# Performance work log

Hardware: AMD Instinct MI355X
Metric: run time of the kernel (lower is better)

The kernel has to match this reference:

```python
import jax, jax.numpy as jnp
import numpy as np

MARGIN = 0.3
HARD_FACTOR = 0.0
EPS = 1e-6


def setup_inputs() -> dict:
    key = jax.random.key(0)
    k1, k2 = jax.random.split(key)
    inputs = jax.random.normal(k1, (4096, 256), dtype=jnp.float32)
    targets = jax.random.randint(k2, (4096,), 0, 512, dtype=jnp.int64)
    return {"inputs": inputs, "targets": targets}


def reference(inputs, targets):
    n = inputs.shape[0]
    half = n // 2
    # L2-normalize features (matches normalize(): x / (||x|| + 1e-6))
    x = inputs / (jnp.linalg.norm(inputs, axis=-1, keepdims=True) + EPS)
    # pairwise euclidean distances, clamped at 1e-6 before sqrt
    sq = jnp.sum(x * x, axis=1)                      # (n,)
    dist = sq[:, None] + sq[None, :] - 2.0 * (x @ x.T)  # (n, n)
    dist = jnp.sqrt(jnp.clip(dist, EPS))
    # same-identity mask
    mask = targets[:, None] == targets[None, :]      # (n, n) bool
    # rows in the first half mine over columns [half:n], rows in the
    # second half mine over columns [0:half] -> gather the opposite half
    first = (jnp.arange(n) < half)[:, None]          # (n, 1)
    d_o = jnp.where(first, dist[:, half:], dist[:, :half])  # (n, half)
    m_o = jnp.where(first, mask[:, half:], mask[:, :half])  # (n, half) bool
    pos_any = jnp.any(m_o, axis=1)
    neg_any = jnp.any(~m_o, axis=1)
    dist_ap = jnp.where(pos_any,
                        jnp.max(jnp.where(m_o, d_o, -jnp.inf), axis=1),
                        0.0)
    dist_an = jnp.where(neg_any,
                        jnp.min(jnp.where(m_o, jnp.inf, d_o), axis=1),
                        1.0)
    dist_ap = dist_ap * (1.0 + HARD_FACTOR)
    dist_an = dist_an * (1.0 - HARD_FACTOR)
    # MarginRankingLoss(margin)(dist_an, dist_ap, y=1) =
    #   mean(relu(-(dist_an - dist_ap) + margin))
    loss = jnp.mean(jax.nn.relu(dist_ap - dist_an + MARGIN))
    return loss
```

## Files before the change

kernel.cpp:

```cpp
#include <hip/hip_runtime.h>
#include <math.h>

#define N 4096
#define D 256
#define HALF 2048
#define MARGIN 0.3f

#define BM 64

typedef __attribute__((ext_vector_type(8))) short bf16x8;
typedef __attribute__((ext_vector_type(4))) float f32x4;

typedef __attribute__((address_space(1))) const unsigned int gas_uint;
typedef __attribute__((address_space(3))) unsigned int las_uint;

__device__ __forceinline__ void gld16(const unsigned short* g, unsigned short* l) {
    __builtin_amdgcn_global_load_lds((gas_uint*)g, (las_uint*)l, 16, 0, 0);
}

__device__ __forceinline__ unsigned short f2bf(float x) {
    unsigned int u = __float_as_uint(x);
    return (unsigned short)((u + 0x7fffu + ((u >> 16) & 1u)) >> 16);
}

__global__ __launch_bounds__(256) void k_norm(const float* __restrict__ in,
                                              unsigned short* __restrict__ xnb,
                                              float* __restrict__ sq,
                                              int* __restrict__ ap,
                                              int* __restrict__ an) {
    const int row = blockIdx.x * 4 + (threadIdx.x >> 6);
    const int lane = threadIdx.x & 63;
    const float4 v = *(const float4*)&in[(size_t)row * D + lane * 4];
    float s = v.x * v.x + v.y * v.y + v.z * v.z + v.w * v.w;
#pragma unroll
    for (int o = 1; o < 64; o <<= 1) s += __shfl_xor(s, o, 64);
    float nrm = sqrtf(s);
    float inv = 1.0f / (nrm + 1e-6f);
    ushort4 o4;
    o4.x = f2bf(v.x * inv);
    o4.y = f2bf(v.y * inv);
    o4.z = f2bf(v.z * inv);
    o4.w = f2bf(v.w * inv);
    *(ushort4*)&xnb[(size_t)row * D + lane * 4] = o4;
    if (lane == 0) {
        float q = nrm * inv;
        sq[row] = q * q;
        ap[row] = 0;
        an[row] = 0x7f800000;
    }
}

__global__ __launch_bounds__(256, 2) void k_tile(const unsigned short* __restrict__ xnb,
                                                 const float* __restrict__ sq,
                                                 const int* __restrict__ tg,
                                                 int* __restrict__ ap,
                                                 int* __restrict__ an) {
    __shared__ unsigned short As[BM * D];
    __shared__ unsigned short Bs[BM * D];

    const int bi = blockIdx.y, bj = blockIdx.x;
    const int I0 = bi * BM;
    const int J0 = bj * BM;
    const int tid = threadIdx.x;
    const int wave = tid >> 6, lane = tid & 63;
    const int wm = wave >> 1, wn = wave & 1;
    const int lrow = lane & 15, lquad = lane >> 4;

    const unsigned short* Ag = xnb + (size_t)I0 * D;
    const unsigned short* Bg = xnb + (size_t)(HALF + J0) * D;

#pragma unroll
    for (int i = 0; i < 8; ++i) {
        const int ch = i * 4 + wave;
        const int e = ch * 64 + lane;
        const int row = e >> 5;
        const int sc = (e & 31) ^ (row & 7);
        gld16(Ag + row * D + sc * 8, &As[ch * 512]);
        gld16(Bg + row * D + sc * 8, &Bs[ch * 512]);
    }
    asm volatile("s_waitcnt vmcnt(0)" ::: "memory");
    __syncthreads();

    f32x4 acc[2][2];
#pragma unroll
    for (int a = 0; a < 2; ++a)
#pragma unroll
        for (int b = 0; b < 2; ++b) acc[a][b] = (f32x4){0.f, 0.f, 0.f, 0.f};

#pragma unroll
    for (int kk = 0; kk < 8; ++kk) {
        bf16x8 af[2], bfr[2];
#pragma unroll
        for (int mi = 0; mi < 2; ++mi) {
            const int r = wm * 32 + mi * 16 + lrow;
            const int s = r * 32 + ((kk * 4 + lquad) ^ (r & 7));
            af[mi] = *(const bf16x8*)&As[s * 8];
        }
#pragma unroll
        for (int nj = 0; nj < 2; ++nj) {
            const int r = wn * 32 + nj * 16 + lrow;
            const int s = r * 32 + ((kk * 4 + lquad) ^ (r & 7));
            bfr[nj] = *(const bf16x8*)&Bs[s * 8];
        }
#pragma unroll
        for (int mi = 0; mi < 2; ++mi)
#pragma unroll
            for (int nj = 0; nj < 2; ++nj)
                acc[mi][nj] = __builtin_amdgcn_mfma_f32_16x16x32_bf16(
                    af[mi], bfr[nj], acc[mi][nj], 0, 0, 0);
    }

    float sqi[2][4], sqj[2];
    int tgi[2][4], tgj[2];
#pragma unroll
    for (int mi = 0; mi < 2; ++mi)
#pragma unroll
        for (int r = 0; r < 4; ++r) {
            int gi = I0 + wm * 32 + mi * 16 + lquad * 4 + r;
            sqi[mi][r] = sq[gi];
            tgi[mi][r] = tg[gi];
        }
#pragma unroll
    for (int nj = 0; nj < 2; ++nj) {
        int gj = HALF + J0 + wn * 32 + nj * 16 + lrow;
        sqj[nj] = sq[gj];
        tgj[nj] = tg[gj];
    }

    const float INF = __int_as_float(0x7f800000);
    float rap[2][4], ran[2][4], capv[2], canv[2];
#pragma unroll
    for (int mi = 0; mi < 2; ++mi)
#pragma unroll
        for (int r = 0; r < 4; ++r) { rap[mi][r] = 0.f; ran[mi][r] = INF; }
#pragma unroll
    for (int nj = 0; nj < 2; ++nj) { capv[nj] = 0.f; canv[nj] = INF; }

#pragma unroll
    for (int mi = 0; mi < 2; ++mi)
#pragma unroll
        for (int nj = 0; nj < 2; ++nj)
#pragma unroll
            for (int r = 0; r < 4; ++r) {
                float d2 = sqi[mi][r] + sqj[nj] - 2.0f * acc[mi][nj][r];
                float d = sqrtf(fmaxf(d2, 1e-6f));
                if (tgi[mi][r] == tgj[nj]) {
                    rap[mi][r] = fmaxf(rap[mi][r], d);
                    capv[nj] = fmaxf(capv[nj], d);
                } else {
                    ran[mi][r] = fminf(ran[mi][r], d);
                    canv[nj] = fminf(canv[nj], d);
                }
            }

#pragma unroll
    for (int mi = 0; mi < 2; ++mi)
#pragma unroll
        for (int r = 0; r < 4; ++r) {
#pragma unroll
            for (int o = 1; o < 16; o <<= 1) {
                rap[mi][r] = fmaxf(rap[mi][r], __shfl_xor(rap[mi][r], o, 64));
                ran[mi][r] = fminf(ran[mi][r], __shfl_xor(ran[mi][r], o, 64));
            }
        }
#pragma unroll
    for (int nj = 0; nj < 2; ++nj) {
#pragma unroll
        for (int o = 16; o < 64; o <<= 1) {
            capv[nj] = fmaxf(capv[nj], __shfl_xor(capv[nj], o, 64));
            canv[nj] = fminf(canv[nj], __shfl_xor(canv[nj], o, 64));
        }
    }

    int* sra = (int*)As;
    int* srn = sra + BM;
    int* sca = srn + BM;
    int* scn = sca + BM;

    __syncthreads();
    if (tid < BM) { sra[tid] = 0; srn[tid] = 0x7f800000;
                    sca[tid] = 0; scn[tid] = 0x7f800000; }
    __syncthreads();
    if (lrow == 0) {
#pragma unroll
        for (int mi = 0; mi < 2; ++mi)
#pragma unroll
            for (int r = 0; r < 4; ++r) {
                int lr = wm * 32 + mi * 16 + lquad * 4 + r;
                atomicMax(&sra[lr], __float_as_int(rap[mi][r]));
                atomicMin(&srn[lr], __float_as_int(ran[mi][r]));
            }
    }
    if (lquad == 0) {
#pragma unroll
        for (int nj = 0; nj < 2; ++nj) {
            int lc = wn * 32 + nj * 16 + lrow;
            atomicMax(&sca[lc], __float_as_int(capv[nj]));
            atomicMin(&scn[lc], __float_as_int(canv[nj]));
        }
    }
    __syncthreads();
    if (tid < BM) {
        atomicMax(&ap[I0 + tid], sra[tid]);
        atomicMin(&an[I0 + tid], srn[tid]);
        atomicMax(&ap[HALF + J0 + tid], sca[tid]);
        atomicMin(&an[HALF + J0 + tid], scn[tid]);
    }
}

__global__ __launch_bounds__(1024) void k_loss(const int* __restrict__ ap,
                                               const int* __restrict__ an,
                                               float* __restrict__ out) {
    const int t = threadIdx.x;
    float s = 0.f;
#pragma unroll
    for (int i = t; i < N; i += 1024) {
        float dap = __int_as_float(ap[i]);
        int anb = an[i];
        float dan = (anb == 0x7f800000) ? 1.0f : __int_as_float(anb);
        float v = dap - dan + MARGIN;
        s += (v > 0.f) ? v : 0.f;
    }
#pragma unroll
    for (int o = 32; o > 0; o >>= 1) s += __shfl_down(s, o, 64);
    __shared__ float wsum[16];
    if ((t & 63) == 0) wsum[t >> 6] = s;
    __syncthreads();
    if (t == 0) {
        float tot = 0.f;
#pragma unroll
        for (int w = 0; w < 16; ++w) tot += wsum[w];
        out[0] = tot / (float)N;
    }
}

extern "C" void kernel_launch(void* const* d_in, const int* in_sizes, int n_in,
                              void* d_out, int out_size, void* d_ws, size_t ws_size,
                              hipStream_t stream) {
    const float* in = (const float*)d_in[0];
    const int* tg = (const int*)d_in[1];
    float* out = (float*)d_out;

    unsigned short* xnb = (unsigned short*)d_ws;
    float* sq = (float*)(xnb + (size_t)N * D);
    int* ap = (int*)(sq + N);
    int* an = ap + N;

    k_norm<<<N / 4, 256, 0, stream>>>(in, xnb, sq, ap, an);
    k_tile<<<dim3(HALF / BM, HALF / BM), 256, 0, stream>>>(xnb, sq, tg, ap, an);
    k_loss<<<1, 1024, 0, stream>>>(ap, an, out);
}
```

Baseline: 73.47 us.

## Fuse norm, tile and loss into one cooperative persistent kernel

Merges the three kernels into one cooperative kernel with 256 persistent blocks separated by grid syncs. Each block processes four tile jobs and writes its per-tile row and column partial max/min into partial buffers instead of using global atomics. A final phase reduces those partials and the per-block loss sums. This removes two kernel launches and global atomic contention, at the cost of grid-sync overhead, larger workspace traffic and fewer concurrent blocks per tile.

```diff
diff --git a/kernel.cpp b/kernel.cpp
--- a/kernel.cpp
+++ b/kernel.cpp
@@ -1,5 +1,8 @@
 #include <hip/hip_runtime.h>
+#include <hip/hip_cooperative_groups.h>
 #include <math.h>
+
+namespace cg = cooperative_groups;
 
 #define N 4096
 #define D 256
@@ -7,6 +10,9 @@
 #define MARGIN 0.3f
 
 #define BM 64
+#define GRID 256
+#define TPB 256
+#define NTJ 32
 
 typedef __attribute__((ext_vector_type(8))) short bf16x8;
 typedef __attribute__((ext_vector_type(4))) float f32x4;
@@ -23,213 +29,231 @@
     return (unsigned short)((u + 0x7fffu + ((u >> 16) & 1u)) >> 16);
 }
 
-__global__ __launch_bounds__(256) void k_norm(const float* __restrict__ in,
-                                              unsigned short* __restrict__ xnb,
-                                              float* __restrict__ sq,
-                                              int* __restrict__ ap,
-                                              int* __restrict__ an) {
-    const int row = blockIdx.x * 4 + (threadIdx.x >> 6);
-    const int lane = threadIdx.x & 63;
-    const float4 v = *(const float4*)&in[(size_t)row * D + lane * 4];
-    float s = v.x * v.x + v.y * v.y + v.z * v.z + v.w * v.w;
-#pragma unroll
-    for (int o = 1; o < 64; o <<= 1) s += __shfl_xor(s, o, 64);
-    float nrm = sqrtf(s);
-    float inv = 1.0f / (nrm + 1e-6f);
-    ushort4 o4;
-    o4.x = f2bf(v.x * inv);
-    o4.y = f2bf(v.y * inv);
-    o4.z = f2bf(v.z * inv);
-    o4.w = f2bf(v.w * inv);
-    *(ushort4*)&xnb[(size_t)row * D + lane * 4] = o4;
-    if (lane == 0) {
-        float q = nrm * inv;
-        sq[row] = q * q;
-        ap[row] = 0;
-        an[row] = 0x7f800000;
-    }
-}
-
-__global__ __launch_bounds__(256, 2) void k_tile(const unsigned short* __restrict__ xnb,
-                                                 const float* __restrict__ sq,
-                                                 const int* __restrict__ tg,
-                                                 int* __restrict__ ap,
-                                                 int* __restrict__ an) {
+__global__ __launch_bounds__(TPB) void k_fused(const float* __restrict__ in,
+                                               const int* __restrict__ tg,
+                                               float* __restrict__ out,
+                                               unsigned short* __restrict__ xnb,
+                                               float* __restrict__ sq,
+                                               int* __restrict__ rp_ap,
+                                               int* __restrict__ rp_an,
+                                               int* __restrict__ cp_ap,
+                                               int* __restrict__ cp_an,
+                                               float* __restrict__ bsum) {
+    cg::grid_group grid = cg::this_grid();
+    const int tid = threadIdx.x;
+    const int wave = tid >> 6, lane = tid & 63;
+
+#pragma unroll
+    for (int r = 0; r < 4; ++r) {
+        const int row = blockIdx.x * 16 + wave * 4 + r;
+        const float4 v = *(const float4*)&in[(size_t)row * D + lane * 4];
+        float s = v.x * v.x + v.y * v.y + v.z * v.z + v.w * v.w;
+#pragma unroll
+        for (int o = 1; o < 64; o <<= 1) s += __shfl_xor(s, o, 64);
+        float nrm = sqrtf(s);
+        float inv = 1.0f / (nrm + 1e-6f);
+        ushort4 o4;
+        o4.x = f2bf(v.x * inv);
+        o4.y = f2bf(v.y * inv);
+        o4.z = f2bf(v.z * inv);
+        o4.w = f2bf(v.w * inv);
+        *(ushort4*)&xnb[(size_t)row * D + lane * 4] = o4;
+        if (lane == 0) {
+            float q = nrm * inv;
+            sq[row] = q * q;
+        }
+    }
+
+    grid.sync();
+
     __shared__ unsigned short As[BM * D];
     __shared__ unsigned short Bs[BM * D];
-
-    const int bi = blockIdx.y, bj = blockIdx.x;
-    const int I0 = bi * BM;
-    const int J0 = bj * BM;
-    const int tid = threadIdx.x;
-    const int wave = tid >> 6, lane = tid & 63;
+    __shared__ int sra[BM], srn[BM], sca[BM], scn[BM];
+
     const int wm = wave >> 1, wn = wave & 1;
     const int lrow = lane & 15, lquad = lane >> 4;
-
-    const unsigned short* Ag = xnb + (size_t)I0 * D;
-    const unsigned short* Bg = xnb + (size_t)(HALF + J0) * D;
-
-#pragma unroll
-    for (int i = 0; i < 8; ++i) {
-        const int ch = i * 4 + wave;
-        const int e = ch * 64 + lane;
-        const int row = e >> 5;
-        const int sc = (e & 31) ^ (row & 7);
-        gld16(Ag + row * D + sc * 8, &As[ch * 512]);
-        gld16(Bg + row * D + sc * 8, &Bs[ch * 512]);
-    }
-    asm volatile("s_waitcnt vmcnt(0)" ::: "memory");
-    __syncthreads();
-
-    f32x4 acc[2][2];
-#pragma unroll
-    for (int a = 0; a < 2; ++a)
-#pragma unroll
-        for (int b = 0; b < 2; ++b) acc[a][b] = (f32x4){0.f, 0.f, 0.f, 0.f};
-
-#pragma unroll
-    for (int kk = 0; kk < 8; ++kk) {
-        bf16x8 af[2], bfr[2];
-#pragma unroll
-        for (int mi = 0; mi < 2; ++mi) {
-            const int r = wm * 32 + mi * 16 + lrow;
-            const int s = r * 32 + ((kk * 4 + lquad) ^ (r & 7));
-            af[mi] = *(const bf16x8*)&As[s * 8];
-        }
+    const float INF = __int_as_float(0x7f800000);
+
+    for (int jt = 0; jt < 4; ++jt) {
+        const int job = jt * GRID + blockIdx.x;
+        const int bi = job >> 5, bj = job & (NTJ - 1);
+        const int I0 = bi * BM;
+        const int J0 = bj * BM;
+        const unsigned short* Ag = xnb + (size_t)I0 * D;
+        const unsigned short* Bg = xnb + (size_t)(HALF + J0) * D;
+
+        __syncthreads();
+#pragma unroll
+        for (int i = 0; i < 8; ++i) {
+            const int ch = i * 4 + wave;
+            const int e = ch * 64 + lane;
+            const int row = e >> 5;
+            const int sc = (e & 31) ^ (row & 7);
+            gld16(Ag + row * D + sc * 8, &As[ch * 512]);
+            gld16(Bg + row * D + sc * 8, &Bs[ch * 512]);
+        }
+        if (tid < BM) {
+            sra[tid] = 0; srn[tid] = 0x7f800000;
+            sca[tid] = 0; scn[tid] = 0x7f800000;
+        }
+        asm volatile("s_waitcnt vmcnt(0)" ::: "memory");
+        __syncthreads();
+
+        f32x4 acc[2][2];
+#pragma unroll
+        for (int a = 0; a < 2; ++a)
+#pragma unroll
+            for (int b = 0; b < 2; ++b) acc[a][b] = (f32x4){0.f, 0.f, 0.f, 0.f};
+
+#pragma unroll
+        for (int kk = 0; kk < 8; ++kk) {
+            bf16x8 af[2], bfr[2];
+#pragma unroll
+            for (int mi = 0; mi < 2; ++mi) {
+                const int r = wm * 32 + mi * 16 + lrow;
+                const int s = r * 32 + ((kk * 4 + lquad) ^ (r & 7));
+                af[mi] = *(const bf16x8*)&As[s * 8];
+            }
+#pragma unroll
+            for (int nj = 0; nj < 2; ++nj) {
+                const int r = wn * 32 + nj * 16 + lrow;
+                const int s = r * 32 + ((kk * 4 + lquad) ^ (r & 7));
+                bfr[nj] = *(const bf16x8*)&Bs[s * 8];
+            }
+#pragma unroll
+            for (int mi = 0; mi < 2; ++mi)
+#pragma unroll
+                for (int nj = 0; nj < 2; ++nj)
+                    acc[mi][nj] = __builtin_amdgcn_mfma_f32_16x16x32_bf16(
+                        af[mi], bfr[nj], acc[mi][nj], 0, 0, 0);
+        }
+
+        float sqi[2][4], sqj[2];
+        int tgi[2][4], tgj[2];
+#pragma unroll
+        for (int mi = 0; mi < 2; ++mi)
+#pragma unroll
+            for (int r = 0; r < 4; ++r) {
+                int gi = I0 + wm * 32 + mi * 16 + lquad * 4 + r;
+                sqi[mi][r] = sq[gi];
+                tgi[mi][r] = tg[gi];
+            }
 #pragma unroll
         for (int nj = 0; nj < 2; ++nj) {
-            const int r = wn * 32 + nj * 16 + lrow;
-            const int s = r * 32 + ((kk * 4 + lquad) ^ (r & 7));
-            bfr[nj] = *(const bf16x8*)&Bs[s * 8];
-        }
+            int gj = HALF + J0 + wn * 32 + nj * 16 + lrow;
+            sqj[nj] = sq[gj];
+            tgj[nj] = tg[gj];
+        }
+
+        float rap[2][4], ran[2][4], capv[2], canv[2];
+#pragma unroll
+        for (int mi = 0; mi < 2; ++mi)
+#pragma unroll
+            for (int r = 0; r < 4; ++r) { rap[mi][r] = 0.f; ran[mi][r] = INF; }
+#pragma unroll
+        for (int nj = 0; nj < 2; ++nj) { capv[nj] = 0.f; canv[nj] = INF; }
+
 #pragma unroll
         for (int mi = 0; mi < 2; ++mi)
 #pragma unroll
             for (int nj = 0; nj < 2; ++nj)
-                acc[mi][nj] = __builtin_amdgcn_mfma_f32_16x16x32_bf16(
-                    af[mi], bfr[nj], acc[mi][nj], 0, 0, 0);
-    }
-
-    float sqi[2][4], sqj[2];
-    int tgi[2][4], tgj[2];
-#pragma unroll
-    for (int mi = 0; mi < 2; ++mi)
-#pragma unroll
-        for (int r = 0; r < 4; ++r) {
-            int gi = I0 + wm * 32 + mi * 16 + lquad * 4 + r;
-            sqi[mi][r] = sq[gi];
-            tgi[mi][r] = tg[gi];
-        }
-#pragma unroll
-    for (int nj = 0; nj < 2; ++nj) {
-        int gj = HALF + J0 + wn * 32 + nj * 16 + lrow;
-        sqj[nj] = sq[gj];
-        tgj[nj] = tg[gj];
-    }
-
-    const float INF = __int_as_float(0x7f800000);
-    float rap[2][4], ran[2][4], capv[2], canv[2];
-#pragma unroll
-    for (int mi = 0; mi < 2; ++mi)
-#pragma unroll
-        for (int r = 0; r < 4; ++r) { rap[mi][r] = 0.f; ran[mi][r] = INF; }
-#pragma unroll
-    for (int nj = 0; nj < 2; ++nj) { capv[nj] = 0.f; canv[nj] = INF; }
-
-#pragma unroll
-    for (int mi = 0; mi < 2; ++mi)
-#pragma unroll
-        for (int nj = 0; nj < 2; ++nj)
+#pragma unroll
+                for (int r = 0; r < 4; ++r) {
+                    float d2 = sqi[mi][r] + sqj[nj] - 2.0f * acc[mi][nj][r];
+                    float d = sqrtf(fmaxf(d2, 1e-6f));
+                    if (tgi[mi][r] == tgj[nj]) {
+                        rap[mi][r] = fmaxf(rap[mi][r], d);
+                        capv[nj] = fmaxf(capv[nj], d);
+                    } else {
+                        ran[mi][r] = fminf(ran[mi][r], d);
+                        canv[nj] = fminf(canv[nj], d);
+                    }
+                }
+
+#pragma unroll
+        for (int mi = 0; mi < 2; ++mi)
 #pragma unroll
             for (int r = 0; r < 4; ++r) {
-                float d2 = sqi[mi][r] + sqj[nj] - 2.0f * acc[mi][nj][r];
-                float d = sqrtf(fmaxf(d2, 1e-6f));
-                if (tgi[mi][r] == tgj[nj]) {
-                    rap[mi][r] = fmaxf(rap[mi][r], d);
-                    capv[nj] = fmaxf(capv[nj], d);
-                } else {
-                    ran[mi][r] = fminf(ran[mi][r], d);
-                    canv[nj] = fminf(canv[nj], d);
+#pragma unroll
+                for (int o = 1; o < 16; o <<= 1) {
+                    rap[mi][r] = fmaxf(rap[mi][r], __shfl_xor(rap[mi][r], o, 64));
+                    ran[mi][r] = fminf(ran[mi][r], __shfl_xor(ran[mi][r], o, 64));
                 }
             }
-
-#pragma unroll
-    for (int mi = 0; mi < 2; ++mi)
-#pragma unroll
-        for (int r = 0; r < 4; ++r) {
-#pragma unroll
-            for (int o = 1; o < 16; o <<= 1) {
-                rap[mi][r] = fmaxf(rap[mi][r], __shfl_xor(rap[mi][r], o, 64));
-                ran[mi][r] = fminf(ran[mi][r], __shfl_xor(ran[mi][r], o, 64));
-            }
-        }
-#pragma unroll
-    for (int nj = 0; nj < 2; ++nj) {
-#pragma unroll
-        for (int o = 16; o < 64; o <<= 1) {
-            capv[nj] = fmaxf(capv[nj], __shfl_xor(capv[nj], o, 64));
-            canv[nj] = fminf(canv[nj], __shfl_xor(canv[nj], o, 64));
-        }
-    }
-
-    int* sra = (int*)As;
-    int* srn = sra + BM;
-    int* sca = srn + BM;
-    int* scn = sca + BM;
-
-    __syncthreads();
-    if (tid < BM) { sra[tid] = 0; srn[tid] = 0x7f800000;
-                    sca[tid] = 0; scn[tid] = 0x7f800000; }
-    __syncthreads();
-    if (lrow == 0) {
-#pragma unroll
-        for (int mi = 0; mi < 2; ++mi)
-#pragma unroll
-            for (int r = 0; r < 4; ++r) {
-                int lr = wm * 32 + mi * 16 + lquad * 4 + r;
-                atomicMax(&sra[lr], __float_as_int(rap[mi][r]));
-                atomicMin(&srn[lr], __float_as_int(ran[mi][r]));
-            }
-    }
-    if (lquad == 0) {
 #pragma unroll
         for (int nj = 0; nj < 2; ++nj) {
-            int lc = wn * 32 + nj * 16 + lrow;
-            atomicMax(&sca[lc], __float_as_int(capv[nj]));
-            atomicMin(&scn[lc], __float_as_int(canv[nj]));
-        }
-    }
-    __syncthreads();
-    if (tid < BM) {
-        atomicMax(&ap[I0 + tid], sra[tid]);
-        atomicMin(&an[I0 + tid], srn[tid]);
-        atomicMax(&ap[HALF + J0 + tid], sca[tid]);
-        atomicMin(&an[HALF + J0 + tid], scn[tid]);
-    }
-}
-
-__global__ __launch_bounds__(1024) void k_loss(const int* __restrict__ ap,
-                                               const int* __restrict__ an,
-                                               float* __restrict__ out) {
-    const int t = threadIdx.x;
-    float s = 0.f;
-#pragma unroll
-    for (int i = t; i < N; i += 1024) {
-        float dap = __int_as_float(ap[i]);
-        int anb = an[i];
+#pragma unroll
+            for (int o = 16; o < 64; o <<= 1) {
+                capv[nj] = fmaxf(capv[nj], __shfl_xor(capv[nj], o, 64));
+                canv[nj] = fminf(canv[nj], __shfl_xor(canv[nj], o, 64));
+            }
+        }
+
+        if (lrow == 0) {
+#pragma unroll
+            for (int mi = 0; mi < 2; ++mi)
+#pragma unroll
+                for (int r = 0; r < 4; ++r) {
+                    int lr = wm * 32 + mi * 16 + lquad * 4 + r;
+                    atomicMax(&sra[lr], __float_as_int(rap[mi][r]));
+                    atomicMin(&srn[lr], __float_as_int(ran[mi][r]));
+                }
+        }
+        if (lquad == 0) {
+#pragma unroll
+            for (int nj = 0; nj < 2; ++nj) {
+                int lc = wn * 32 + nj * 16 + lrow;
+                atomicMax(&sca[lc], __float_as_int(capv[nj]));
+                atomicMin(&scn[lc], __float_as_int(canv[nj]));
+            }
+        }
+        __syncthreads();
+        if (tid < BM) {
+            rp_ap[bj * HALF + I0 + tid] = sra[tid];
+            rp_an[bj * HALF + I0 + tid] = srn[tid];
+            cp_ap[bi * HALF + J0 + tid] = sca[tid];
+            cp_an[bi * HALF + J0 + tid] = scn[tid];
+        }
+    }
+
+    grid.sync();
+
+    if (blockIdx.x < 16) {
+        const int i = blockIdx.x * TPB + tid;
+        int apb = 0, anb = 0x7f800000;
+        if (i < HALF) {
+#pragma unroll 8
+            for (int b = 0; b < NTJ; ++b) {
+                apb = max(apb, rp_ap[b * HALF + i]);
+                anb = min(anb, rp_an[b * HALF + i]);
+            }
+        } else {
+            const int j = i - HALF;
+#pragma unroll 8
+            for (int b = 0; b < NTJ; ++b) {
+                apb = max(apb, cp_ap[b * HALF + j]);
+                anb = min(anb, cp_an[b * HALF + j]);
+            }
+        }
+        float dap = __int_as_float(apb);
         float dan = (anb == 0x7f800000) ? 1.0f : __int_as_float(anb);
         float v = dap - dan + MARGIN;
-        s += (v > 0.f) ? v : 0.f;
-    }
-#pragma unroll
-    for (int o = 32; o > 0; o >>= 1) s += __shfl_down(s, o, 64);
-    __shared__ float wsum[16];
-    if ((t & 63) == 0) wsum[t >> 6] = s;
-    __syncthreads();
-    if (t == 0) {
+        float part = (v > 0.f) ? v : 0.f;
+#pragma unroll
+        for (int o = 1; o < 64; o <<= 1) part += __shfl_xor(part, o, 64);
+        __shared__ float fsum[4];
+        if (lane == 0) fsum[wave] = part;
+        __syncthreads();
+        if (tid == 0)
+            bsum[blockIdx.x] = fsum[0] + fsum[1] + fsum[2] + fsum[3];
+    }
+
+    grid.sync();
+
+    if (blockIdx.x == 0 && tid == 0) {
         float tot = 0.f;
 #pragma unroll
-        for (int w = 0; w < 16; ++w) tot += wsum[w];
+        for (int b = 0; b < 16; ++b) tot += bsum[b];
         out[0] = tot / (float)N;
     }
 }
@@ -243,10 +267,14 @@
 
     unsigned short* xnb = (unsigned short*)d_ws;
     float* sq = (float*)(xnb + (size_t)N * D);
-    int* ap = (int*)(sq + N);
-    int* an = ap + N;
-
-    k_norm<<<N / 4, 256, 0, stream>>>(in, xnb, sq, ap, an);
-    k_tile<<<dim3(HALF / BM, HALF / BM), 256, 0, stream>>>(xnb, sq, tg, ap, an);
-    k_loss<<<1, 1024, 0, stream>>>(ap, an, out);
-}
+    int* rp_ap = (int*)(sq + N);
+    int* rp_an = rp_ap + NTJ * HALF;
+    int* cp_ap = rp_an + NTJ * HALF;
+    int* cp_an = cp_ap + NTJ * HALF;
+    float* bsum = (float*)(cp_an + NTJ * HALF);
+
+    void* args[] = {&in, &tg, &out, &xnb, &sq,
+                    &rp_ap, &rp_an, &cp_ap, &cp_an, &bsum};
+    hipLaunchCooperativeKernel((void*)k_fused, dim3(GRID), dim3(TPB),
+                               args, 0, stream);
+}
```

Result: slower. 170.6 us (+132.2%).

## Fuse final loss reduction into tile kernel via per-strip completion counters

Applied to the files above, without the earlier changes.

Removes the separate single-block loss kernel. Each tile block bumps a per-row-strip and per-column-strip counter, and the last block to finish a strip sums the hinge loss for its 64 rows into a slot. A global counter then lets the last strip finisher add up all the slots and write the mean. The reduction scratch also moves to dedicated shared arrays, which drops two barriers. This saves one kernel launch and its serial tail, at the cost of extra atomics, fences and counter-reset logic that depends on self-resetting global counters.

```diff
diff --git a/kernel.cpp b/kernel.cpp
--- a/kernel.cpp
+++ b/kernel.cpp
@@ -7,12 +7,17 @@
 #define MARGIN 0.3f
 
 #define BM 64
+#define NTJ 32
 
 typedef __attribute__((ext_vector_type(8))) short bf16x8;
 typedef __attribute__((ext_vector_type(4))) float f32x4;
 
 typedef __attribute__((address_space(1))) const unsigned int gas_uint;
 typedef __attribute__((address_space(3))) unsigned int las_uint;
+
+__device__ unsigned int g_row_cnt[NTJ];
+__device__ unsigned int g_col_cnt[NTJ];
+__device__ unsigned int g_fin_cnt;
 
 __device__ __forceinline__ void gld16(const unsigned short* g, unsigned short* l) {
     __builtin_amdgcn_global_load_lds((gas_uint*)g, (las_uint*)l, 16, 0, 0);
@@ -54,9 +59,12 @@
                                                  const float* __restrict__ sq,
                                                  const int* __restrict__ tg,
                                                  int* __restrict__ ap,
-                                                 int* __restrict__ an) {
+                                                 int* __restrict__ an,
+                                                 float* __restrict__ strip_sum,
+                                                 float* __restrict__ out) {
     __shared__ unsigned short As[BM * D];
     __shared__ unsigned short Bs[BM * D];
+    __shared__ int sra[BM], srn[BM], sca[BM], scn[BM];
 
     const int bi = blockIdx.y, bj = blockIdx.x;
     const int I0 = bi * BM;
@@ -77,6 +85,10 @@
         const int sc = (e & 31) ^ (row & 7);
         gld16(Ag + row * D + sc * 8, &As[ch * 512]);
         gld16(Bg + row * D + sc * 8, &Bs[ch * 512]);
+    }
+    if (tid < BM) {
+        sra[tid] = 0; srn[tid] = 0x7f800000;
+        sca[tid] = 0; scn[tid] = 0x7f800000;
     }
     asm volatile("s_waitcnt vmcnt(0)" ::: "memory");
     __syncthreads();
@@ -172,15 +184,6 @@
         }
     }
 
-    int* sra = (int*)As;
-    int* srn = sra + BM;
-    int* sca = srn + BM;
-    int* scn = sca + BM;
-
-    __syncthreads();
-    if (tid < BM) { sra[tid] = 0; srn[tid] = 0x7f800000;
-                    sca[tid] = 0; scn[tid] = 0x7f800000; }
-    __syncthreads();
     if (lrow == 0) {
 #pragma unroll
         for (int mi = 0; mi < 2; ++mi)
@@ -206,31 +209,54 @@
         atomicMax(&ap[HALF + J0 + tid], sca[tid]);
         atomicMin(&an[HALF + J0 + tid], scn[tid]);
     }
-}
-
-__global__ __launch_bounds__(1024) void k_loss(const int* __restrict__ ap,
-                                               const int* __restrict__ an,
-                                               float* __restrict__ out) {
-    const int t = threadIdx.x;
-    float s = 0.f;
-#pragma unroll
-    for (int i = t; i < N; i += 1024) {
-        float dap = __int_as_float(ap[i]);
-        int anb = an[i];
-        float dan = (anb == 0x7f800000) ? 1.0f : __int_as_float(anb);
-        float v = dap - dan + MARGIN;
-        s += (v > 0.f) ? v : 0.f;
-    }
-#pragma unroll
-    for (int o = 32; o > 0; o >>= 1) s += __shfl_down(s, o, 64);
-    __shared__ float wsum[16];
-    if ((t & 63) == 0) wsum[t >> 6] = s;
+    __threadfence();
     __syncthreads();
-    if (t == 0) {
-        float tot = 0.f;
-#pragma unroll
-        for (int w = 0; w < 16; ++w) tot += wsum[w];
-        out[0] = tot / (float)N;
+
+    if (wave < 2) {
+        unsigned int* cnt = (wave == 0) ? &g_row_cnt[bi] : &g_col_cnt[bj];
+        const int base = (wave == 0) ? I0 : HALF + J0;
+        const int slot = (wave == 0) ? bi : NTJ + bj;
+        int fin = 0;
+        if (lane == 0) {
+            unsigned int old = __hip_atomic_fetch_add(
+                cnt, 1u, __ATOMIC_ACQ_REL, __HIP_MEMORY_SCOPE_AGENT);
+            fin = (old == NTJ - 1);
+            if (fin)
+                __hip_atomic_fetch_add(cnt, 0u - (unsigned)NTJ,
+                                       __ATOMIC_RELAXED, __HIP_MEMORY_SCOPE_AGENT);
+        }
+        fin = __shfl(fin, 0, 64);
+        if (fin) {
+            __threadfence();
+            int apb = __hip_atomic_load(&ap[base + lane],
+                        __ATOMIC_RELAXED, __HIP_MEMORY_SCOPE_AGENT);
+            int anb = __hip_atomic_load(&an[base + lane],
+                        __ATOMIC_RELAXED, __HIP_MEMORY_SCOPE_AGENT);
+            float dap = __int_as_float(apb);
+            float dan = (anb == 0x7f800000) ? 1.0f : __int_as_float(anb);
+            float v = dap - dan + MARGIN;
+            float sl = (v > 0.f) ? v : 0.f;
+#pragma unroll
+            for (int o = 1; o < 64; o <<= 1) sl += __shfl_xor(sl, o, 64);
+            if (lane == 0) {
+                __hip_atomic_store(&strip_sum[slot], sl,
+                                   __ATOMIC_RELAXED, __HIP_MEMORY_SCOPE_AGENT);
+                __threadfence();
+                unsigned int fo = __hip_atomic_fetch_add(
+                    &g_fin_cnt, 1u, __ATOMIC_ACQ_REL, __HIP_MEMORY_SCOPE_AGENT);
+                if (fo == 2u * NTJ - 1u) {
+                    __hip_atomic_fetch_add(&g_fin_cnt, 0u - 2u * (unsigned)NTJ,
+                                           __ATOMIC_RELAXED, __HIP_MEMORY_SCOPE_AGENT);
+                    __threadfence();
+                    float tot = 0.f;
+#pragma unroll
+                    for (int b = 0; b < 2 * NTJ; ++b)
+                        tot += __hip_atomic_load(&strip_sum[b],
+                                 __ATOMIC_RELAXED, __HIP_MEMORY_SCOPE_AGENT);
+                    out[0] = tot / (float)N;
+                }
+            }
+        }
     }
 }
 
@@ -245,8 +271,9 @@
     float* sq = (float*)(xnb + (size_t)N * D);
     int* ap = (int*)(sq + N);
     int* an = ap + N;
+    float* strip_sum = (float*)(an + N);
 
     k_norm<<<N / 4, 256, 0, stream>>>(in, xnb, sq, ap, an);
-    k_tile<<<dim3(HALF / BM, HALF / BM), 256, 0, stream>>>(xnb, sq, tg, ap, an);
-    k_loss<<<1, 1024, 0, stream>>>(ap, an, out);
-}
+    k_tile<<<dim3(NTJ, NTJ), 256, 0, stream>>>(xnb, sq, tg, ap, an,
+                                               strip_sum, out);
+}
```

Result: slower. 164.8 us (+124.3%).
